# Performance work log

Hardware: AMD Instinct MI355X
Metric: run time of the kernel (lower is better)

The kernel has to match this reference:

```python
import jax, jax.numpy as jnp
import numpy as np

L2_REG = 0.02


def setup_inputs() -> dict:
    key = jax.random.key(0)
    k1, k2 = jax.random.split(key)
    n, d = 4096, 1024
    anchors = jax.random.normal(k1, (n, d), dtype=jnp.float32)
    positives = jax.random.normal(k2, (n, d), dtype=jnp.float32)
    return {"anchors": anchors, "positives": positives}


def reference(anchors, positives):
    # Fused equivalent of the per-row masked_select loop:
    # x[i, j] = a_i . (p_j - p_i) = S[i, j] - S[i, i], for j != i
    n = anchors.shape[0]
    S = anchors @ positives.T                     # (n, n)
    x = S - jnp.diag(S)[:, None]                  # subtract anchor-positive sim per row
    offdiag = ~jnp.eye(n, dtype=bool)
    # sum over negatives j != i of exp(x[i, j])
    s = jnp.sum(jnp.where(offdiag, jnp.exp(x), 0.0), axis=1)  # (n,)
    n_pair = jnp.mean(jnp.log1p(s))
    l2 = jnp.sum(anchors ** 2 + positives ** 2) / n
    return n_pair + L2_REG * l2
```

## Files before the change

kernel.cpp:

```cpp
#include <hip/hip_runtime.h>
#include <math.h>
#include <stdint.h>

#define N 4096
#define Dm 1024
#define BK 64
#define NT (Dm / BK)
#define NCB (N / 64)
#define NPART 512

typedef __attribute__((ext_vector_type(8))) short bf16x8;
typedef __attribute__((ext_vector_type(4))) float f32x4;

typedef const void __attribute__((address_space(1)))* gas_t;
typedef void __attribute__((address_space(3)))* las_t;

static __device__ __forceinline__ void gload_lds16(const void* g, void* l) {
    __builtin_amdgcn_global_load_lds((gas_t)g, (las_t)l, 16, 0, 0);
}

static __device__ __forceinline__ unsigned short f2bf(float f) {
    unsigned int u = __float_as_uint(f);
    unsigned int r = (u + 0x7fff + ((u >> 16) & 1)) >> 16;
    return (unsigned short)r;
}

__global__ __launch_bounds__(256) void prep_kernel(const float* __restrict__ A,
                                                   const float* __restrict__ P,
                                                   unsigned short* __restrict__ Abf,
                                                   unsigned short* __restrict__ Pbf,
                                                   float* __restrict__ D,
                                                   float* __restrict__ rowl2,
                                                   float* __restrict__ accL,
                                                   float* __restrict__ accR,
                                                   unsigned int* __restrict__ ticket) {
    if (blockIdx.x == 0 && threadIdx.x == 0) {
        accL[0] = 0.0f; accR[0] = 0.0f; ticket[0] = 0u;
    }
    int t = threadIdx.x;
    int lane = t & 63;
    int row = blockIdx.x * 4 + (t >> 6);
    const float4* a4 = (const float4*)(A + (size_t)row * Dm);
    const float4* p4 = (const float4*)(P + (size_t)row * Dm);
    ushort4* ao = (ushort4*)(Abf + (size_t)row * Dm);
    ushort4* po = (ushort4*)(Pbf + (size_t)row * Dm);
    float dot = 0.0f, l2 = 0.0f;
#pragma unroll
    for (int c = 0; c < 4; ++c) {
        int idx = c * 64 + lane;
        float4 a = a4[idx], p = p4[idx];
        ushort4 ab, pb;
        ab.x = f2bf(a.x); ab.y = f2bf(a.y); ab.z = f2bf(a.z); ab.w = f2bf(a.w);
        pb.x = f2bf(p.x); pb.y = f2bf(p.y); pb.z = f2bf(p.z); pb.w = f2bf(p.w);
        ao[idx] = ab; po[idx] = pb;
        dot += a.x * p.x + a.y * p.y + a.z * p.z + a.w * p.w;
        l2  += a.x * a.x + a.y * a.y + a.z * a.z + a.w * a.w
             + p.x * p.x + p.y * p.y + p.z * p.z + p.w * p.w;
    }
#pragma unroll
    for (int off = 32; off; off >>= 1) {
        dot += __shfl_xor(dot, off, 64);
        l2  += __shfl_xor(l2,  off, 64);
    }
    if (lane == 0) {
        D[row]     = dot;
        rowl2[row] = l2;
    }
}

#define STAGE_TILE(gp, lp, kt) do {                                            \
        gload_lds16((gp) + (kt),                    (lp)         + tid * 8);   \
        gload_lds16((gp) + (kt) +  64 * (size_t)Dm, (lp) + 4096  + tid * 8);   \
        gload_lds16((gp) + (kt) + 128 * (size_t)Dm, (lp) + 8192  + tid * 8);   \
        gload_lds16((gp) + (kt) + 192 * (size_t)Dm, (lp) + 12288 + tid * 8);   \
    } while (0)

#define STAGE_B_HALF(lpB, kt, h) do {                                          \
        gload_lds16(gB + (kt) + ((h) ? 128 * (size_t)Dm : (size_t)0),          \
                    (lpB) + (h) * 8192 + tid * 8);                             \
        gload_lds16(gB + (kt) + ((h) ? 192 * (size_t)Dm : 64 * (size_t)Dm),    \
                    (lpB) + (h) * 8192 + 4096 + tid * 8);                      \
    } while (0)

#define READ_A4(dst, buf, rg0) do {                                            \
        dst[0] = *(const bf16x8*)((buf) + ((rg0)     * 16) * BK + aoff0);      \
        dst[1] = *(const bf16x8*)((buf) + ((rg0)     * 16) * BK + aoff1);      \
        dst[2] = *(const bf16x8*)((buf) + ((rg0) + 1) * 16 * BK + aoff0);      \
        dst[3] = *(const bf16x8*)((buf) + ((rg0) + 1) * 16 * BK + aoff1);      \
    } while (0)

#define READ_B8(buf) do {                                                      \
        _Pragma("unroll")                                                      \
        for (int j = 0; j < 4; ++j) {                                          \
            bfr[j][0] = *(const bf16x8*)((buf) + j * 16 * BK + aoff0);         \
            bfr[j][1] = *(const bf16x8*)((buf) + j * 16 * BK + aoff1);         \
        }                                                                      \
    } while (0)

#define MFMA_PH(P, ap)                                                         \
    _Pragma("unroll")                                                          \
    for (int j = 0; j < 4; ++j)                                                \
        acc[2*(P)][j]   = __builtin_amdgcn_mfma_f32_16x16x32_bf16(ap[0], bfr[j][0], acc[2*(P)][j],   0, 0, 0); \
    _Pragma("unroll")                                                          \
    for (int j = 0; j < 4; ++j)                                                \
        acc[2*(P)][j]   = __builtin_amdgcn_mfma_f32_16x16x32_bf16(ap[1], bfr[j][1], acc[2*(P)][j],   0, 0, 0); \
    _Pragma("unroll")                                                          \
    for (int j = 0; j < 4; ++j)                                                \
        acc[2*(P)+1][j] = __builtin_amdgcn_mfma_f32_16x16x32_bf16(ap[2], bfr[j][0], acc[2*(P)+1][j], 0, 0, 0); \
    _Pragma("unroll")                                                          \
    for (int j = 0; j < 4; ++j)                                                \
        acc[2*(P)+1][j] = __builtin_amdgcn_mfma_f32_16x16x32_bf16(ap[3], bfr[j][1], acc[2*(P)+1][j], 0, 0, 0);

#define PHASE_EDGE() do {                                                      \
        __builtin_amdgcn_sched_barrier(0);                                     \
        __builtin_amdgcn_s_barrier();                                          \
        asm volatile("s_waitcnt lgkmcnt(0)" ::: "memory");                     \
        __builtin_amdgcn_sched_barrier(0);                                     \
    } while (0)

#define TILE_BODY(CUR, NXT) do {                                               \
        const unsigned short* aT  = aBase + (CUR) * 16384;                     \
        const unsigned short* aTn = aBase + (NXT) * 16384;                     \
        const unsigned short* bTn = bBase + (NXT) * 16384;                     \
        unsigned short* stA = &As[NXT][0];                                     \
        unsigned short* stB = &Bs[CUR][0];                                     \
           \
        READ_A4(aF[1], aT, 2);                                                 \
        if (t >= 1 && t <= 14) STAGE_TILE(gA, stA, (t + 1) * BK);              \
        __builtin_amdgcn_s_setprio(1);                                         \
        MFMA_PH(0, aF[0])                                                      \
        __builtin_amdgcn_s_setprio(0);                                         \
        PHASE_EDGE();                                                          \
             \
        READ_A4(aF[0], aT, 4);                                                 \
        if (t <= 13) STAGE_B_HALF(stB, (t + 2) * BK, 0);                       \
        __builtin_amdgcn_s_setprio(1);                                         \
        MFMA_PH(1, aF[1])                                                      \
        __builtin_amdgcn_s_setprio(0);                                         \
        PHASE_EDGE();                                                          \
             \
        READ_A4(aF[1], aT, 6);                                                 \
        if (t <= 13) STAGE_B_HALF(stB, (t + 2) * BK, 1);                       \
        __builtin_amdgcn_s_setprio(1);                                         \
        MFMA_PH(2, aF[0])                                                      \
        __builtin_amdgcn_s_setprio(0);                                         \
        PHASE_EDGE();                                                          \
        \
        __builtin_amdgcn_s_setprio(1);                                         \
        MFMA_PH(3, aF[1])                                                      \
        __builtin_amdgcn_s_setprio(0);                                         \
        __builtin_amdgcn_sched_barrier(0);                                     \
        if (t <= 13)      { asm volatile("s_waitcnt vmcnt(4)" ::: "memory"); } \
        else if (t == 14) { asm volatile("s_waitcnt vmcnt(0)" ::: "memory"); } \
        if (t <= 14) {                                                         \
            __builtin_amdgcn_s_barrier();                                      \
            READ_B8(bTn);                                                      \
            READ_A4(aF[0], aTn, 0);                                            \
            PHASE_EDGE();                                                      \
        }                                                                      \
    } while (0)

__global__ __launch_bounds__(512, 2) void npair_mfma(const unsigned short* __restrict__ Abf,
                                                     const unsigned short* __restrict__ Pbf,
                                                     float* __restrict__ Mpart,
                                                     float* __restrict__ Spart) {
    __shared__ unsigned short As[2][256 * BK];
    __shared__ unsigned short Bs[2][256 * BK];

    int tid = threadIdx.x;
    int lane = tid & 63;
    int wid = tid >> 6;
    int wr = wid >> 2, wc = wid & 3;

    int bid = blockIdx.y * gridDim.x + blockIdx.x;
    int xcd = bid & 7, lid = bid >> 3;
    int by = (xcd >> 1) * 4 + (lid >> 3);
    int bx = (xcd & 1) * 8 + (lid & 7);
    int row0 = by * 256, col0 = bx * 256;

    int srow = tid >> 3;
    int kcol = (tid & 7) ^ (srow & 7);
    const unsigned short* gA = Abf + (size_t)(row0 + srow) * Dm + (kcol << 3);
    const unsigned short* gB = Pbf + (size_t)(col0 + srow) * Dm + (kcol << 3);

    STAGE_TILE(gA, &As[0][0], 0);
    STAGE_TILE(gB, &Bs[0][0], 0);
    STAGE_TILE(gA, &As[1][0], BK);
    STAGE_TILE(gB, &Bs[1][0], BK);
    asm volatile("s_waitcnt vmcnt(8)" ::: "memory");
    __builtin_amdgcn_s_barrier();

    int l15 = lane & 15;
    int aoff0 = (((lane >> 4)    ) ^ (lane & 7)) << 3;
    int aoff1 = (((lane >> 4) + 4) ^ (lane & 7)) << 3;
    const unsigned short* aBase = &As[0][0] + (wr * 128 + l15) * BK;
    const unsigned short* bBase = &Bs[0][0] + (wc * 64  + l15) * BK;

    f32x4 acc[8][4] = {};
    bf16x8 bfr[4][2];
    bf16x8 aF[2][4];

    READ_B8(bBase);
    READ_A4(aF[0], aBase, 0);
    __builtin_amdgcn_sched_barrier(0);
    asm volatile("s_waitcnt lgkmcnt(0)" ::: "memory");
    __builtin_amdgcn_sched_barrier(0);

    for (int tt = 0; tt < NT / 2; ++tt) {
        int t = 2 * tt;
        TILE_BODY(0, 1);
        t = 2 * tt + 1;
        TILE_BODY(1, 0);
    }

    __builtin_amdgcn_sched_barrier(0);

    int cb = bx * 4 + wc;
#pragma unroll
    for (int i = 0; i < 8; ++i) {
        int rloc = wr * 128 + i * 16 + ((lane >> 4) << 2);
#pragma unroll
        for (int e = 0; e < 4; ++e) {
            int gr = row0 + rloc + e;
            float xs[4];
            float m = -INFINITY;
#pragma unroll
            for (int j = 0; j < 4; ++j) {
                int gc = col0 + wc * 64 + j * 16 + (lane & 15);
                float x = acc[i][j][e];
                if (gr == gc) x = -INFINITY;
                xs[j] = x;
                m = fmaxf(m, x);
            }
#pragma unroll
            for (int off = 8; off; off >>= 1) m = fmaxf(m, __shfl_xor(m, off, 64));
            float s = 0.0f;
#pragma unroll
            for (int j = 0; j < 4; ++j) s += __expf(xs[j] - m);
#pragma unroll
            for (int off = 8; off; off >>= 1) s += __shfl_xor(s, off, 64);
            if ((lane & 15) == 0) {
                Mpart[(size_t)gr * NCB + cb] = m;
                Spart[(size_t)gr * NCB + cb] = s;
            }
        }
    }
}

__global__ __launch_bounds__(256) void combine_final(const float* __restrict__ Mpart,
                                                     const float* __restrict__ Spart,
                                                     const float* __restrict__ D,
                                                     const float* __restrict__ rowl2,
                                                     float* __restrict__ accL,
                                                     float* __restrict__ accR,
                                                     unsigned int* __restrict__ ticket,
                                                     float* __restrict__ out) {
    int t = threadIdx.x;
    int lane = t & 63;
    int w = t >> 6;
    __shared__ float ls[8];
#pragma unroll
    for (int r = 0; r < 2; ++r) {
        int row = blockIdx.x * 8 + w * 2 + r;
        float mp = Mpart[(size_t)row * NCB + lane];
        float sp = Spart[(size_t)row * NCB + lane];
        float m = mp;
#pragma unroll
        for (int off = 32; off; off >>= 1) m = fmaxf(m, __shfl_xor(m, off, 64));
        float s = sp * __expf(mp - m);
#pragma unroll
        for (int off = 32; off; off >>= 1) s += __shfl_xor(s, off, 64);
        if (lane == 0) {
            float z = m + logf(s) - D[row];
            ls[w * 2 + r] = fmaxf(z, 0.0f) + log1pf(__expf(-fabsf(z)));
        }
    }
    __syncthreads();
    if (t == 0) {
        int r8 = blockIdx.x * 8;
        float L = 0.0f, R = 0.0f;
#pragma unroll
        for (int r = 0; r < 8; ++r) { L += ls[r]; R += rowl2[r8 + r]; }
        atomicAdd(accL, L);
        atomicAdd(accR, R);
        __threadfence();
        unsigned int done = atomicAdd(ticket, 1u);
        if (done == NPART - 1) {
            float aL = atomicAdd(accL, 0.0f);
            float aR = atomicAdd(accR, 0.0f);
            out[0] = aL / (float)N + 0.02f * (aR / (float)N);
        }
    }
}

extern "C" void kernel_launch(void* const* d_in, const int* in_sizes, int n_in,
                              void* d_out, int out_size, void* d_ws, size_t ws_size,
                              hipStream_t stream) {
    const float* A = (const float*)d_in[0];
    const float* P = (const float*)d_in[1];
    float* out = (float*)d_out;

    unsigned short* Abf = (unsigned short*)d_ws;
    unsigned short* Pbf = Abf + (size_t)N * Dm;
    float* D     = (float*)(Pbf + (size_t)N * Dm);
    float* rowl2 = D + N;
    float* accL  = rowl2 + N;
    float* accR  = accL + 1;
    unsigned int* ticket = (unsigned int*)(accR + 1);
    float* Mpart = (float*)(ticket + 1);
    float* Spart = Mpart + (size_t)N * NCB;

    prep_kernel<<<N / 4, 256, 0, stream>>>(A, P, Abf, Pbf, D, rowl2, accL, accR, ticket);
    dim3 grid(16, 16);
    npair_mfma<<<grid, 512, 0, stream>>>(Abf, Pbf, Mpart, Spart);
    combine_final<<<N / 8, 256, 0, stream>>>(Mpart, Spart, D, rowl2, accL, accR, ticket, out);
}
```

Baseline: 136.3 us.

## Restructure GEMM main loop into two large MFMA clusters per K-tile

Replaces the four-phase-per-tile schedule, with its fine-grained A/B half staging and many barriers, by a simpler loop. Each K-tile now reads all B fragments and half the A fragments, runs a 32-MFMA cluster, then reads the other half of A and runs a second cluster. A prefetch is one tile ahead and B prefetch two tiles ahead. The aim is fewer barriers and LDS waits per tile and longer uninterrupted MFMA runs, at the cost of more fragment registers and less interleaving of LDS reads with MFMA work.

```diff
diff --git a/kernel.cpp b/kernel.cpp
--- a/kernel.cpp
+++ b/kernel.cpp
@@ -75,20 +75,6 @@
         gload_lds16((gp) + (kt) + 192 * (size_t)Dm, (lp) + 12288 + tid * 8);   \
     } while (0)
 
-#define STAGE_B_HALF(lpB, kt, h) do {                                          \
-        gload_lds16(gB + (kt) + ((h) ? 128 * (size_t)Dm : (size_t)0),          \
-                    (lpB) + (h) * 8192 + tid * 8);                             \
-        gload_lds16(gB + (kt) + ((h) ? 192 * (size_t)Dm : 64 * (size_t)Dm),    \
-                    (lpB) + (h) * 8192 + 4096 + tid * 8);                      \
-    } while (0)
-
-#define READ_A4(dst, buf, rg0) do {                                            \
-        dst[0] = *(const bf16x8*)((buf) + ((rg0)     * 16) * BK + aoff0);      \
-        dst[1] = *(const bf16x8*)((buf) + ((rg0)     * 16) * BK + aoff1);      \
-        dst[2] = *(const bf16x8*)((buf) + ((rg0) + 1) * 16 * BK + aoff0);      \
-        dst[3] = *(const bf16x8*)((buf) + ((rg0) + 1) * 16 * BK + aoff1);      \
-    } while (0)
-
 #define READ_B8(buf) do {                                                      \
         _Pragma("unroll")                                                      \
         for (int j = 0; j < 4; ++j) {                                          \
@@ -97,68 +83,23 @@
         }                                                                      \
     } while (0)
 
-#define MFMA_PH(P, ap)                                                         \
-    _Pragma("unroll")                                                          \
-    for (int j = 0; j < 4; ++j)                                                \
-        acc[2*(P)][j]   = __builtin_amdgcn_mfma_f32_16x16x32_bf16(ap[0], bfr[j][0], acc[2*(P)][j],   0, 0, 0); \
-    _Pragma("unroll")                                                          \
-    for (int j = 0; j < 4; ++j)                                                \
-        acc[2*(P)][j]   = __builtin_amdgcn_mfma_f32_16x16x32_bf16(ap[1], bfr[j][1], acc[2*(P)][j],   0, 0, 0); \
-    _Pragma("unroll")                                                          \
-    for (int j = 0; j < 4; ++j)                                                \
-        acc[2*(P)+1][j] = __builtin_amdgcn_mfma_f32_16x16x32_bf16(ap[2], bfr[j][0], acc[2*(P)+1][j], 0, 0, 0); \
-    _Pragma("unroll")                                                          \
-    for (int j = 0; j < 4; ++j)                                                \
-        acc[2*(P)+1][j] = __builtin_amdgcn_mfma_f32_16x16x32_bf16(ap[3], bfr[j][1], acc[2*(P)+1][j], 0, 0, 0);
-
-#define PHASE_EDGE() do {                                                      \
-        __builtin_amdgcn_sched_barrier(0);                                     \
-        __builtin_amdgcn_s_barrier();                                          \
-        asm volatile("s_waitcnt lgkmcnt(0)" ::: "memory");                     \
-        __builtin_amdgcn_sched_barrier(0);                                     \
-    } while (0)
-
-#define TILE_BODY(CUR, NXT) do {                                               \
-        const unsigned short* aT  = aBase + (CUR) * 16384;                     \
-        const unsigned short* aTn = aBase + (NXT) * 16384;                     \
-        const unsigned short* bTn = bBase + (NXT) * 16384;                     \
-        unsigned short* stA = &As[NXT][0];                                     \
-        unsigned short* stB = &Bs[CUR][0];                                     \
-           \
-        READ_A4(aF[1], aT, 2);                                                 \
-        if (t >= 1 && t <= 14) STAGE_TILE(gA, stA, (t + 1) * BK);              \
-        __builtin_amdgcn_s_setprio(1);                                         \
-        MFMA_PH(0, aF[0])                                                      \
-        __builtin_amdgcn_s_setprio(0);                                         \
-        PHASE_EDGE();                                                          \
-             \
-        READ_A4(aF[0], aT, 4);                                                 \
-        if (t <= 13) STAGE_B_HALF(stB, (t + 2) * BK, 0);                       \
-        __builtin_amdgcn_s_setprio(1);                                         \
-        MFMA_PH(1, aF[1])                                                      \
-        __builtin_amdgcn_s_setprio(0);                                         \
-        PHASE_EDGE();                                                          \
-             \
-        READ_A4(aF[1], aT, 6);                                                 \
-        if (t <= 13) STAGE_B_HALF(stB, (t + 2) * BK, 1);                       \
-        __builtin_amdgcn_s_setprio(1);                                         \
-        MFMA_PH(2, aF[0])                                                      \
-        __builtin_amdgcn_s_setprio(0);                                         \
-        PHASE_EDGE();                                                          \
-        \
-        __builtin_amdgcn_s_setprio(1);                                         \
-        MFMA_PH(3, aF[1])                                                      \
-        __builtin_amdgcn_s_setprio(0);                                         \
-        __builtin_amdgcn_sched_barrier(0);                                     \
-        if (t <= 13)      { asm volatile("s_waitcnt vmcnt(4)" ::: "memory"); } \
-        else if (t == 14) { asm volatile("s_waitcnt vmcnt(0)" ::: "memory"); } \
-        if (t <= 14) {                                                         \
-            __builtin_amdgcn_s_barrier();                                      \
-            READ_B8(bTn);                                                      \
-            READ_A4(aF[0], aTn, 0);                                            \
-            PHASE_EDGE();                                                      \
+#define READ_A8(buf, rg0) do {                                                 \
+        _Pragma("unroll")                                                      \
+        for (int r = 0; r < 4; ++r) {                                          \
+            aF[2*r]   = *(const bf16x8*)((buf) + (((rg0)+r) * 16) * BK + aoff0); \
+            aF[2*r+1] = *(const bf16x8*)((buf) + (((rg0)+r) * 16) * BK + aoff1); \
         }                                                                      \
     } while (0)
+
+#define MFMA_CLUSTER(accbase)                                                  \
+    _Pragma("unroll")                                                          \
+    for (int r = 0; r < 4; ++r)                                                \
+        _Pragma("unroll")                                                      \
+        for (int ks = 0; ks < 2; ++ks)                                         \
+            _Pragma("unroll")                                                  \
+            for (int j = 0; j < 4; ++j)                                        \
+                acc[(accbase)+r][j] = __builtin_amdgcn_mfma_f32_16x16x32_bf16( \
+                    aF[2*r+ks], bfr[j][ks], acc[(accbase)+r][j], 0, 0, 0);
 
 __global__ __launch_bounds__(512, 2) void npair_mfma(const unsigned short* __restrict__ Abf,
                                                      const unsigned short* __restrict__ Pbf,
@@ -185,10 +126,7 @@
 
     STAGE_TILE(gA, &As[0][0], 0);
     STAGE_TILE(gB, &Bs[0][0], 0);
-    STAGE_TILE(gA, &As[1][0], BK);
     STAGE_TILE(gB, &Bs[1][0], BK);
-    asm volatile("s_waitcnt vmcnt(8)" ::: "memory");
-    __builtin_amdgcn_s_barrier();
 
     int l15 = lane & 15;
     int aoff0 = (((lane >> 4)    ) ^ (lane & 7)) << 3;
@@ -198,19 +136,42 @@
 
     f32x4 acc[8][4] = {};
     bf16x8 bfr[4][2];
-    bf16x8 aF[2][4];
-
-    READ_B8(bBase);
-    READ_A4(aF[0], aBase, 0);
-    __builtin_amdgcn_sched_barrier(0);
-    asm volatile("s_waitcnt lgkmcnt(0)" ::: "memory");
-    __builtin_amdgcn_sched_barrier(0);
-
-    for (int tt = 0; tt < NT / 2; ++tt) {
-        int t = 2 * tt;
-        TILE_BODY(0, 1);
-        t = 2 * tt + 1;
-        TILE_BODY(1, 0);
+    bf16x8 aF[8];
+
+    for (int t = 0; t < NT; ++t) {
+        const unsigned short* aT = aBase + (t & 1) * 16384;
+        const unsigned short* bT = bBase + (t & 1) * 16384;
+        unsigned short* stA = &As[(t + 1) & 1][0];
+        unsigned short* stB = &Bs[t & 1][0];
+
+        if (t <= 14) { asm volatile("s_waitcnt vmcnt(4)" ::: "memory"); }
+        else         { asm volatile("s_waitcnt vmcnt(0)" ::: "memory"); }
+        __builtin_amdgcn_s_barrier();
+        __builtin_amdgcn_sched_barrier(0);
+
+        READ_B8(bT);
+        READ_A8(aT, 0);
+        if (t <= 14) STAGE_TILE(gA, stA, (t + 1) * BK);
+        __builtin_amdgcn_sched_barrier(0);
+        asm volatile("s_waitcnt lgkmcnt(0)" ::: "memory");
+        __builtin_amdgcn_sched_barrier(0);
+        __builtin_amdgcn_s_setprio(1);
+        MFMA_CLUSTER(0)
+        __builtin_amdgcn_s_setprio(0);
+
+        READ_A8(aT, 4);
+        __builtin_amdgcn_sched_barrier(0);
+        __builtin_amdgcn_s_barrier();
+        __builtin_amdgcn_sched_barrier(0);
+        if (t <= 13) {
+            STAGE_TILE(gB, stB, (t + 2) * BK);
+        }
+        asm volatile("s_waitcnt lgkmcnt(0)" ::: "memory");
+        __builtin_amdgcn_sched_barrier(0);
+        __builtin_amdgcn_s_setprio(1);
+        MFMA_CLUSTER(4)
+        __builtin_amdgcn_s_setprio(0);
+        __builtin_amdgcn_sched_barrier(0);
     }
 
     __builtin_amdgcn_sched_barrier(0);
```

After: 135.0 us. Within noise of the previous version (-1.0%).
